# Kernel tuning notes

Measured on AMD Instinct MI355X. Metric: run time of the kernel, lower is better.

The kernel has to match this reference:

```python
import jax, jax.numpy as jnp
import numpy as np

D_MODEL = 1024
H = 16
D_K = D_MODEL // H


def setup_inputs() -> dict:
    key = jax.random.key(0)
    ks = jax.random.split(key, 12)
    B, S = 2, 2048
    q = jax.random.normal(ks[0], (B, S, D_MODEL), dtype=jnp.float32)
    k = jax.random.normal(ks[1], (B, S, D_MODEL), dtype=jnp.float32)
    v = jax.random.normal(ks[2], (B, S, D_MODEL), dtype=jnp.float32)
    mask = jax.random.randint(ks[3], (1, 1, S, S), 0, 2, dtype=jnp.int32)
    sc = 1.0 / np.sqrt(D_MODEL)
    wq = jax.random.uniform(ks[4], (D_MODEL, D_MODEL), jnp.float32, -sc, sc)
    bq = jax.random.uniform(ks[5], (D_MODEL,), jnp.float32, -sc, sc)
    wk = jax.random.uniform(ks[6], (D_MODEL, D_MODEL), jnp.float32, -sc, sc)
    bk = jax.random.uniform(ks[7], (D_MODEL,), jnp.float32, -sc, sc)
    wv = jax.random.uniform(ks[8], (D_MODEL, D_MODEL), jnp.float32, -sc, sc)
    bv = jax.random.uniform(ks[9], (D_MODEL,), jnp.float32, -sc, sc)
    wo = jax.random.uniform(ks[10], (D_MODEL, D_MODEL), jnp.float32, -sc, sc)
    bo = jax.random.uniform(ks[11], (D_MODEL,), jnp.float32, -sc, sc)
    return {"q": q, "k": k, "v": v, "mask": mask,
            "wq": wq, "bq": bq, "wk": wk, "bk": bk,
            "wv": wv, "bv": bv, "wo": wo, "bo": bo}


def reference(q, k, v, mask, wq, bq, wk, bk, wv, bv, wo, bo):
    B, S, _ = q.shape
    # linear projections (torch Linear: x @ W.T + b)
    query = q @ wq.T + bq
    key = k @ wk.T + bk
    value = v @ wv.T + bv
    # [B, S, D] -> [B, H, S, d_k]
    query = query.reshape(B, S, H, D_K).transpose(0, 2, 1, 3)
    key = key.reshape(B, S, H, D_K).transpose(0, 2, 1, 3)
    value = value.reshape(B, S, H, D_K).transpose(0, 2, 1, 3)
    scores = jnp.einsum('bhqd,bhkd->bhqk', query, key) / jnp.sqrt(
        jnp.asarray(D_K, query.dtype))
    # NOTE: source uses `-1 ** 9` which is -1 in Python, not -1e9 (soft mask)
    scores = jnp.where(mask == 0, jnp.asarray(-1.0, scores.dtype), scores)
    attn = jax.nn.softmax(scores, axis=-1)
    # source calls dropout(attn) but discards the result -> no-op
    x = jnp.einsum('bhqk,bhkd->bhqd', attn, value)
    x = x.transpose(0, 2, 1, 3).reshape(B, S, H * D_K)
    return x @ wo.T + bo
```

## Files before the change

kernel.cpp:

```cpp
#include <hip/hip_runtime.h>
#include <hip/hip_bf16.h>

#define D_MODEL 1024
#define NH 16
#define DK 64
#define S_LEN 2048
#define BATCH 2
#define M_ROWS (BATCH * S_LEN)

typedef float    floatx4 __attribute__((ext_vector_type(4)));
typedef _Float16 half8   __attribute__((ext_vector_type(8)));
typedef _Float16 half4v  __attribute__((ext_vector_type(4)));

#define LOG2E 1.4426950408889634f
#define EXPM1 0.36787944117144233f

__device__ __forceinline__ half8 ldh8(const _Float16* p) {
    return __builtin_bit_cast(half8, *(const uint4*)p);
}
__device__ __forceinline__ void gld16(const void* g, void* l) {
    __builtin_amdgcn_global_load_lds(
        (const __attribute__((address_space(1))) void*)g,
        (__attribute__((address_space(3))) void*)l, 16, 0, 0);
}
__device__ __forceinline__ float dpp_swap1(float x) {
    return __builtin_bit_cast(float,
        __builtin_amdgcn_mov_dpp(__builtin_bit_cast(int, x), 0xB1, 0xF, 0xF, false));
}
__device__ __forceinline__ void rawbar() {
    __builtin_amdgcn_sched_barrier(0);
    __builtin_amdgcn_s_barrier();
    __builtin_amdgcn_sched_barrier(0);
}

__global__ __launch_bounds__(256)
void cast_h(const float* __restrict__ s0, const float* __restrict__ s1,
            const float* __restrict__ s2, const float* __restrict__ s3,
            _Float16* __restrict__ out, int R) {
    const int z = blockIdx.y;
    const float* src = (z == 0) ? s0 : (z == 1) ? s1 : (z == 2) ? s2 : s3;
    const size_t idx = ((size_t)blockIdx.x * 256 + threadIdx.x) * 4;
    float4 v = *(const float4*)&src[idx];
    half4v h = {(_Float16)v.x, (_Float16)v.y, (_Float16)v.z, (_Float16)v.w};
    *(half4v*)&out[(size_t)z * R * 1024 + idx] = h;
}

template <int OUTMODE>
__global__ __launch_bounds__(256)
void gemm_f16(const _Float16* __restrict__ Abase, const _Float16* __restrict__ Wbase,
              const float* __restrict__ b0, const float* __restrict__ b1,
              const float* __restrict__ b2, void* __restrict__ Obase,
              void* __restrict__ Obase2) {
    __shared__ __align__(16) _Float16 As[128 * 64];
    __shared__ __align__(16) _Float16 Ws[128 * 64];
    const int tid = threadIdx.x;
    const int w = tid >> 6, lane = tid & 63;
    const int l15 = lane & 15, q4 = lane >> 4;
    const int z = (OUTMODE == 1) ? blockIdx.z : 0;
    const int m0 = blockIdx.y * 128, n0 = blockIdx.x * 128;
    const int wm = w >> 1, wn = w & 1;

    const _Float16* A = Abase + (size_t)z * M_ROWS * 1024;
    const _Float16* W = Wbase + (size_t)z * 1024 * 1024;
    const float* bias = (OUTMODE == 1) ? ((z == 0) ? b0 : (z == 1) ? b1 : b2) : b0;

    int srow[4], sseg[4];
#pragma unroll
    for (int i = 0; i < 4; i++) {
        const int slot = i * 256 + tid;
        srow[i] = slot >> 3;
        sseg[i] = ((slot & 7) ^ (srow[i] & 7)) * 8;
    }

    int aoff[4][2], woff[4][2];
#pragma unroll
    for (int r = 0; r < 4; r++) {
        const int ar = wm * 64 + r * 16 + l15;
        const int wr = wn * 64 + r * 16 + l15;
#pragma unroll
        for (int kc = 0; kc < 2; kc++) {
            aoff[r][kc] = (ar * 8 + ((kc * 4 + q4) ^ (ar & 7))) * 8;
            woff[r][kc] = (wr * 8 + ((kc * 4 + q4) ^ (wr & 7))) * 8;
        }
    }

    floatx4 acc[4][4];
#pragma unroll
    for (int r = 0; r < 4; r++)
#pragma unroll
        for (int c = 0; c < 4; c++) acc[r][c] = (floatx4){0.f, 0.f, 0.f, 0.f};

    for (int k0 = 0; k0 < 1024; k0 += 64) {
#pragma unroll
        for (int i = 0; i < 4; i++) {
            const int lb = (i * 256 + w * 64) * 8;
            gld16(&A[(size_t)(m0 + srow[i]) * 1024 + k0 + sseg[i]], &As[lb]);
            gld16(&W[(size_t)(n0 + srow[i]) * 1024 + k0 + sseg[i]], &Ws[lb]);
        }
        __syncthreads();

        half8 af[4][2], wf[4][2];
#pragma unroll
        for (int r = 0; r < 4; r++)
#pragma unroll
            for (int kc = 0; kc < 2; kc++) {
                af[r][kc] = ldh8(&As[aoff[r][kc]]);
                wf[r][kc] = ldh8(&Ws[woff[r][kc]]);
            }
#pragma unroll
        for (int kc = 0; kc < 2; kc++)
#pragma unroll
            for (int r = 0; r < 4; r++)
#pragma unroll
                for (int c = 0; c < 4; c++)
                    acc[r][c] = __builtin_amdgcn_mfma_f32_16x16x32_f16(
                        af[r][kc], wf[c][kc], acc[r][c], 0, 0, 0);
        __syncthreads();
    }

#pragma unroll
    for (int r = 0; r < 4; r++)
#pragma unroll
        for (int c = 0; c < 4; c++) {
            const int n = n0 + wn * 64 + c * 16 + l15;
            const int mbase = m0 + wm * 64 + r * 16 + q4 * 4;
            float vals[4];
#pragma unroll
            for (int reg = 0; reg < 4; reg++) vals[reg] = acc[r][c][reg] + bias[n];

            if (OUTMODE == 0) {
#pragma unroll
                for (int reg = 0; reg < 4; reg++)
                    ((float*)Obase)[(size_t)(mbase + reg) * 1024 + n] = vals[reg];
            } else if (z == 2) {
                const int b = mbase >> 11, s = mbase & 2047;
                const int h = n >> 6, d = n & 63;
                half4v hv = {(_Float16)vals[0], (_Float16)vals[1],
                             (_Float16)vals[2], (_Float16)vals[3]};
                *(half4v*)&((_Float16*)Obase2)[
                    (((size_t)((b * 16 + h) * 64 + d)) << 11) + s] = hv;
            } else {
#pragma unroll
                for (int reg = 0; reg < 4; reg++) {
                    const int m = mbase + reg;
                    float val = vals[reg];
                    if (z == 0) val *= 0.125f * LOG2E;
                    const int b = m >> 11, s = m & 2047;
                    const int h = n >> 6, d = n & 63;
                    _Float16* Oz = (_Float16*)Obase + (size_t)z * M_ROWS * 1024;
                    Oz[(((size_t)(b * 16 + h) * S_LEN + s) << 6) + d] = (_Float16)val;
                }
            }
        }
}

__global__ __launch_bounds__(256)
void mask_pack(const int* __restrict__ mask, unsigned long long* __restrict__ mb) {
    const int gw = blockIdx.x * 4 + (threadIdx.x >> 6);
    const int lane = threadIdx.x & 63;
    const int row = gw >> 5, wid = gw & 31;
    const int mv = mask[(size_t)row * S_LEN + wid * 64 + lane];
    unsigned long long bal = __ballot(mv != 0);
    if (lane == 0) mb[gw] = bal;
}

__global__ __launch_bounds__(512, 4)
void attn_mfma(const _Float16* __restrict__ Qh, const _Float16* __restrict__ Kh,
               const _Float16* __restrict__ Vt, const unsigned long long* __restrict__ mb,
               _Float16* __restrict__ Xh) {
    __shared__ __align__(16) _Float16 Ks[2][64 * 64];
    __shared__ __align__(16) _Float16 Vs[2][64 * 64];
    __shared__ __align__(16) _Float16 Ps[8][32 * 72];

    const int tid = threadIdx.x;
    const int w = tid >> 6, lane = tid & 63;
    const int z = w >> 2, w4 = w & 3;
    const int t255 = tid & 255;
    const int l15 = lane & 15, q4 = lane >> 4;
    const int bh = blockIdx.y, b = bh >> 4, h = bh & 15;
    const int qb = blockIdx.x * 128 + w4 * 32;
    const int kbase = z * 1024;

    const _Float16* Qg = Qh + ((size_t)bh * S_LEN + qb) * DK;
    const _Float16* Kg = Kh + ((size_t)bh * S_LEN + kbase) * DK;
    const _Float16* Vg = Vt + (size_t)bh * DK * S_LEN + kbase;

    half8 Aq[2][2];
#pragma unroll
    for (int qs = 0; qs < 2; qs++)
#pragma unroll
        for (int ch = 0; ch < 2; ch++)
            Aq[qs][ch] = ldh8(&Qg[(qs * 16 + l15) * DK + ch * 32 + q4 * 8]);

    int grow[2], gseg[2];
#pragma unroll
    for (int i = 0; i < 2; i++) {
        const int slot = i * 256 + t255;
        grow[i] = slot >> 3;
        gseg[i] = ((slot & 7) ^ (grow[i] & 7)) * 8;
    }

    int kb[2];
#pragma unroll
    for (int ch = 0; ch < 2; ch++)
        kb[ch] = l15 * 64 + (((ch * 4 + q4) ^ (l15 & 7)) * 8);

    const unsigned long long* mrow_p = mb + (size_t)(qb + q4 * 4) * (S_LEN / 64) + z * 16;

    floatx4 O[2][4];
#pragma unroll
    for (int qs = 0; qs < 2; qs++)
#pragma unroll
        for (int nt = 0; nt < 4; nt++) O[qs][nt] = (floatx4){0.f, 0.f, 0.f, 0.f};
    floatx4 lacc[2];
    lacc[0] = (floatx4){0.f, 0.f, 0.f, 0.f};
    lacc[1] = (floatx4){0.f, 0.f, 0.f, 0.f};

    half8 onesB;
#pragma unroll
    for (int i = 0; i < 8; i++) onesB[i] = (_Float16)1.0f;

    const bool evenlane = ((lane & 1) == 0);

#pragma unroll
    for (int i = 0; i < 2; i++) {
        const int lb = (i * 256 + w4 * 64) * 8;
        gld16(&Kg[(size_t)grow[i] * DK + gseg[i]], &Ks[z][lb]);
    }
#pragma unroll
    for (int i = 0; i < 2; i++) {
        const int lb = (i * 256 + w4 * 64) * 8;
        gld16(&Vg[(size_t)grow[i] * S_LEN + gseg[i]], &Vs[z][lb]);
    }

    for (int j0 = 0; j0 < 1024; j0 += 64) {
        const int jn = (j0 + 64) & 1023;
        const int jw = j0 >> 6;

        __builtin_amdgcn_sched_barrier(0);
        asm volatile("s_waitcnt vmcnt(2)" ::: "memory");
        rawbar();

#pragma unroll
        for (int qs = 0; qs < 2; qs++) {
            unsigned long long mw[4];
#pragma unroll
            for (int jt = 0; jt < 4; jt++) {
                floatx4 c = (floatx4){0.f, 0.f, 0.f, 0.f};
                c = __builtin_amdgcn_mfma_f32_16x16x32_f16(
                    Aq[qs][0], ldh8(&Ks[z][jt * 1024 + kb[0]]), c, 0, 0, 0);
                c = __builtin_amdgcn_mfma_f32_16x16x32_f16(
                    Aq[qs][1], ldh8(&Ks[z][jt * 1024 + kb[1]]), c, 0, 0, 0);
                if (jt == 0) {
#pragma unroll
                    for (int reg = 0; reg < 4; reg++)
                        mw[reg] = mrow_p[qs * 512 + reg * 32 + jw];
                }
#pragma unroll
                for (int reg = 0; reg < 4; reg++) {
                    const unsigned ttw =
                        (unsigned)(mw[reg] >> (jt >= 2 ? 32 : 0)) >> l15;
                    const unsigned sel = ttw & (1u << ((jt & 1) * 16));
                    float p = __builtin_amdgcn_exp2f(c[reg]);
                    p = sel ? p : EXPM1;
                    const float po = dpp_swap1(p);
                    if (evenlane) {
                        *(unsigned*)&Ps[w][(qs * 16 + q4 * 4 + reg) * 72 +
                                           jt * 16 + l15] =
                            __builtin_bit_cast(unsigned,
                                __builtin_amdgcn_cvt_pkrtz(p, po));
                    }
                }
            }
        }

        rawbar();
#pragma unroll
        for (int i = 0; i < 2; i++) {
            const int lb = (i * 256 + w4 * 64) * 8;
            gld16(&Kg[(size_t)(jn + grow[i]) * DK + gseg[i]], &Ks[z][lb]);
        }

        __builtin_amdgcn_sched_barrier(0);
        asm volatile("s_waitcnt vmcnt(2)" ::: "memory");
        rawbar();

#pragma unroll
        for (int qs = 0; qs < 2; qs++) {
            half8 Ap[2];
#pragma unroll
            for (int ch = 0; ch < 2; ch++)
                Ap[ch] = ldh8(&Ps[w][(qs * 16 + l15) * 72 + ch * 32 + q4 * 8]);
            lacc[qs] = __builtin_amdgcn_mfma_f32_16x16x32_f16(Ap[0], onesB, lacc[qs], 0, 0, 0);
            lacc[qs] = __builtin_amdgcn_mfma_f32_16x16x32_f16(Ap[1], onesB, lacc[qs], 0, 0, 0);
#pragma unroll
            for (int nt = 0; nt < 4; nt++) {
                O[qs][nt] = __builtin_amdgcn_mfma_f32_16x16x32_f16(
                    Ap[0], ldh8(&Vs[z][nt * 1024 + kb[0]]), O[qs][nt], 0, 0, 0);
                O[qs][nt] = __builtin_amdgcn_mfma_f32_16x16x32_f16(
                    Ap[1], ldh8(&Vs[z][nt * 1024 + kb[1]]), O[qs][nt], 0, 0, 0);
            }
        }

        rawbar();
#pragma unroll
        for (int i = 0; i < 2; i++) {
            const int lb = (i * 256 + w4 * 64) * 8;
            gld16(&Vg[(size_t)grow[i] * S_LEN + jn + gseg[i]], &Vs[z][lb]);
        }
    }
    __builtin_amdgcn_sched_barrier(0);

    float* Obuf = (float*)&Ps[0][0];
    if (z == 1) {
#pragma unroll
        for (int qs = 0; qs < 2; qs++)
#pragma unroll
            for (int reg = 0; reg < 4; reg++) {
                const int rl = w4 * 32 + qs * 16 + q4 * 4 + reg;
#pragma unroll
                for (int nt = 0; nt < 4; nt++)
                    Obuf[rl * 65 + nt * 16 + l15] = O[qs][nt][reg];
                if (l15 == 0) Obuf[rl * 65 + 64] = lacc[qs][reg];
            }
    }
    __syncthreads();
    if (z == 0) {
#pragma unroll
        for (int qs = 0; qs < 2; qs++)
#pragma unroll
            for (int reg = 0; reg < 4; reg++) {
                const int rl = w4 * 32 + qs * 16 + q4 * 4 + reg;
                const float inv = 1.0f / (lacc[qs][reg] + Obuf[rl * 65 + 64]);
                const int srow = qb + qs * 16 + q4 * 4 + reg;
                _Float16* Xrow = Xh + (size_t)(b * S_LEN + srow) * 1024 + h * DK;
#pragma unroll
                for (int nt = 0; nt < 4; nt++)
                    Xrow[nt * 16 + l15] =
                        (_Float16)((O[qs][nt][reg] + Obuf[rl * 65 + nt * 16 + l15]) * inv);
            }
    }
}

extern "C" void kernel_launch(void* const* d_in, const int* in_sizes, int n_in,
                              void* d_out, int out_size, void* d_ws, size_t ws_size,
                              hipStream_t stream) {
    const float* q  = (const float*)d_in[0];
    const float* k  = (const float*)d_in[1];
    const float* v  = (const float*)d_in[2];
    const int* mask = (const int*)d_in[3];
    const float* wq = (const float*)d_in[4];
    const float* bq = (const float*)d_in[5];
    const float* wk = (const float*)d_in[6];
    const float* bk = (const float*)d_in[7];
    const float* wv = (const float*)d_in[8];
    const float* bv = (const float*)d_in[9];
    const float* wo = (const float*)d_in[10];
    const float* bo = (const float*)d_in[11];
    float* out = (float*)d_out;

    char* ws = (char*)d_ws;
    const size_t MB = 1u << 20;
    _Float16* Wh   = (_Float16*)ws;
    _Float16* Ah   = (_Float16*)(ws + 8 * MB);
    _Float16* QKVh = (_Float16*)(ws + 32 * MB);
    _Float16* Vt   = (_Float16*)(ws + 56 * MB);
    unsigned long long* mb = (unsigned long long*)(ws + 64 * MB);
    _Float16* Xh   = Ah;

    cast_h<<<dim3(1024, 4), 256, 0, stream>>>(wq, wk, wv, wo, Wh, 1024);
    cast_h<<<dim3(4096, 3), 256, 0, stream>>>(q, k, v, nullptr, Ah, M_ROWS);

    gemm_f16<1><<<dim3(8, 32, 3), 256, 0, stream>>>(Ah, Wh, bq, bk, bv, QKVh, Vt);

    mask_pack<<<S_LEN * (S_LEN / 64) / 4, 256, 0, stream>>>(mask, mb);

    attn_mfma<<<dim3(16, 32), 512, 0, stream>>>(QKVh, QKVh + (size_t)M_ROWS * 1024,
                                                Vt, mb, Xh);

    gemm_f16<0><<<dim3(8, 32, 1), 256, 0, stream>>>(Xh, Wh + (size_t)3 * 1024 * 1024,
                                                    bo, bo, bo, out, nullptr);
}
```

Measured before the change: 284.9 us.

## Fuse casts and mask packing into one prep kernel; stage GEMM epilogue through LDS

After: 270.7 us. 5.0% less time.

```diff
diff --git a/kernel.cpp b/kernel.cpp
--- a/kernel.cpp
+++ b/kernel.cpp
@@ -34,15 +34,34 @@
 }
 
 __global__ __launch_bounds__(256)
-void cast_h(const float* __restrict__ s0, const float* __restrict__ s1,
-            const float* __restrict__ s2, const float* __restrict__ s3,
-            _Float16* __restrict__ out, int R) {
-    const int z = blockIdx.y;
-    const float* src = (z == 0) ? s0 : (z == 1) ? s1 : (z == 2) ? s2 : s3;
-    const size_t idx = ((size_t)blockIdx.x * 256 + threadIdx.x) * 4;
-    float4 v = *(const float4*)&src[idx];
-    half4v h = {(_Float16)v.x, (_Float16)v.y, (_Float16)v.z, (_Float16)v.w};
-    *(half4v*)&out[(size_t)z * R * 1024 + idx] = h;
+void prep(const float* __restrict__ q, const float* __restrict__ k,
+          const float* __restrict__ v, const float* __restrict__ wq,
+          const float* __restrict__ wk, const float* __restrict__ wv,
+          const float* __restrict__ wo, const int* __restrict__ mask,
+          _Float16* __restrict__ Ah, _Float16* __restrict__ Wh,
+          unsigned long long* __restrict__ mb) {
+    const int y = blockIdx.y;
+    if (y < 7) {
+        if (y >= 3 && blockIdx.x >= 1024) return;
+        const float* src = (y == 0) ? q : (y == 1) ? k : (y == 2) ? v :
+                           (y == 3) ? wq : (y == 4) ? wk : (y == 5) ? wv : wo;
+        _Float16* dst = (y < 3) ? (Ah + (size_t)y * M_ROWS * 1024)
+                                : (Wh + (size_t)(y - 3) * 1024 * 1024);
+        const size_t idx = ((size_t)blockIdx.x * 256 + threadIdx.x) * 4;
+        float4 f = *(const float4*)&src[idx];
+        half4v h = {(_Float16)f.x, (_Float16)f.y, (_Float16)f.z, (_Float16)f.w};
+        *(half4v*)&dst[idx] = h;
+    } else {
+        const int wv_ = threadIdx.x >> 6, lane = threadIdx.x & 63;
+#pragma unroll
+        for (int i = 0; i < 4; i++) {
+            const int gw = blockIdx.x * 16 + wv_ * 4 + i;
+            const int row = gw >> 5, wid = gw & 31;
+            const int mv = mask[(size_t)row * S_LEN + wid * 64 + lane];
+            unsigned long long bal = __ballot(mv != 0);
+            if (lane == 0) mb[gw] = bal;
+        }
+    }
 }
 
 template <int OUTMODE>
@@ -51,8 +70,9 @@
               const float* __restrict__ b0, const float* __restrict__ b1,
               const float* __restrict__ b2, void* __restrict__ Obase,
               void* __restrict__ Obase2) {
-    __shared__ __align__(16) _Float16 As[128 * 64];
-    __shared__ __align__(16) _Float16 Ws[128 * 64];
+    __shared__ __align__(16) _Float16 SM[16384];
+    _Float16* As = SM;
+    _Float16* Ws = SM + 8192;
     const int tid = threadIdx.x;
     const int w = tid >> 6, lane = tid & 63;
     const int l15 = lane & 15, q4 = lane >> 4;
@@ -118,50 +138,77 @@
         __syncthreads();
     }
 
-#pragma unroll
-    for (int r = 0; r < 4; r++)
-#pragma unroll
-        for (int c = 0; c < 4; c++) {
-            const int n = n0 + wn * 64 + c * 16 + l15;
-            const int mbase = m0 + wm * 64 + r * 16 + q4 * 4;
-            float vals[4];
-#pragma unroll
-            for (int reg = 0; reg < 4; reg++) vals[reg] = acc[r][c][reg] + bias[n];
-
-            if (OUTMODE == 0) {
+    if (OUTMODE == 0) {
+#pragma unroll
+        for (int r = 0; r < 4; r++)
+#pragma unroll
+            for (int c = 0; c < 4; c++) {
+                const int n = n0 + wn * 64 + c * 16 + l15;
+                const int mbase = m0 + wm * 64 + r * 16 + q4 * 4;
 #pragma unroll
                 for (int reg = 0; reg < 4; reg++)
-                    ((float*)Obase)[(size_t)(mbase + reg) * 1024 + n] = vals[reg];
-            } else if (z == 2) {
-                const int b = mbase >> 11, s = mbase & 2047;
-                const int h = n >> 6, d = n & 63;
-                half4v hv = {(_Float16)vals[0], (_Float16)vals[1],
-                             (_Float16)vals[2], (_Float16)vals[3]};
-                *(half4v*)&((_Float16*)Obase2)[
-                    (((size_t)((b * 16 + h) * 64 + d)) << 11) + s] = hv;
-            } else {
-#pragma unroll
-                for (int reg = 0; reg < 4; reg++) {
-                    const int m = mbase + reg;
-                    float val = vals[reg];
-                    if (z == 0) val *= 0.125f * LOG2E;
-                    const int b = m >> 11, s = m & 2047;
-                    const int h = n >> 6, d = n & 63;
-                    _Float16* Oz = (_Float16*)Obase + (size_t)z * M_ROWS * 1024;
-                    Oz[(((size_t)(b * 16 + h) * S_LEN + s) << 6) + d] = (_Float16)val;
+                    ((float*)Obase)[(size_t)(mbase + reg) * 1024 + n] =
+                        acc[r][c][reg] + bias[n];
+            }
+    } else {
+        const int h0 = n0 >> 6;
+        const int bB = m0 >> 11;
+        if (z == 2) {
+#pragma unroll
+            for (int r = 0; r < 4; r++)
+#pragma unroll
+                for (int c = 0; c < 4; c++) {
+                    const int nl = wn * 64 + c * 16 + l15;
+                    const int ml = wm * 64 + r * 16 + q4 * 4;
+                    half4v hv;
+#pragma unroll
+                    for (int reg = 0; reg < 4; reg++)
+                        hv[reg] = (_Float16)(acc[r][c][reg] + bias[n0 + nl]);
+                    const int seg = ml >> 3, wi = ml & 7;
+                    *(half4v*)&SM[nl * 128 + ((seg ^ (nl & 7)) << 3) + wi] = hv;
                 }
-            }
-        }
-}
-
-__global__ __launch_bounds__(256)
-void mask_pack(const int* __restrict__ mask, unsigned long long* __restrict__ mb) {
-    const int gw = blockIdx.x * 4 + (threadIdx.x >> 6);
-    const int lane = threadIdx.x & 63;
-    const int row = gw >> 5, wid = gw & 31;
-    const int mv = mask[(size_t)row * S_LEN + wid * 64 + lane];
-    unsigned long long bal = __ballot(mv != 0);
-    if (lane == 0) mb[gw] = bal;
+            __syncthreads();
+#pragma unroll
+            for (int it = 0; it < 8; it++) {
+                const int chunk = it * 256 + tid;
+                const int row = chunk >> 4, seg = chunk & 15;
+                half8 v8 = ldh8(&SM[row * 128 + ((seg ^ (row & 7)) << 3)]);
+                const int d = row & 63, hh = row >> 6;
+                const int s = (m0 & 2047) + seg * 8;
+                *(uint4*)&((_Float16*)Obase2)[
+                    (((size_t)((bB * 16 + h0 + hh) * 64 + d)) << 11) + s] =
+                    __builtin_bit_cast(uint4, v8);
+            }
+        } else {
+            const float sc = (z == 0) ? 0.125f * LOG2E : 1.0f;
+#pragma unroll
+            for (int r = 0; r < 4; r++)
+#pragma unroll
+                for (int c = 0; c < 4; c++) {
+                    const int nl = wn * 64 + c * 16 + l15;
+                    const int seg = nl >> 3, wi = nl & 7;
+                    const float bv = bias[n0 + nl];
+#pragma unroll
+                    for (int reg = 0; reg < 4; reg++) {
+                        const int ml = wm * 64 + r * 16 + q4 * 4 + reg;
+                        SM[ml * 128 + ((seg ^ (ml & 7)) << 3) + wi] =
+                            (_Float16)((acc[r][c][reg] + bv) * sc);
+                    }
+                }
+            __syncthreads();
+            _Float16* Oz = (_Float16*)Obase + (size_t)z * M_ROWS * 1024;
+#pragma unroll
+            for (int it = 0; it < 8; it++) {
+                const int chunk = it * 256 + tid;
+                const int row = chunk >> 4, seg = chunk & 15;
+                half8 v8 = ldh8(&SM[row * 128 + ((seg ^ (row & 7)) << 3)]);
+                const int s = (m0 + row) & 2047;
+                const int hh = seg >> 3, d = (seg & 7) * 8;
+                *(uint4*)&Oz[(((size_t)((bB * 16 + h0 + hh)) * S_LEN + s) << 6) + d] =
+                    __builtin_bit_cast(uint4, v8);
+            }
+        }
+    }
 }
 
 __global__ __launch_bounds__(512, 4)
@@ -247,10 +294,12 @@
 #pragma unroll
             for (int jt = 0; jt < 4; jt++) {
                 floatx4 c = (floatx4){0.f, 0.f, 0.f, 0.f};
+                __builtin_amdgcn_s_setprio(1);
                 c = __builtin_amdgcn_mfma_f32_16x16x32_f16(
                     Aq[qs][0], ldh8(&Ks[z][jt * 1024 + kb[0]]), c, 0, 0, 0);
                 c = __builtin_amdgcn_mfma_f32_16x16x32_f16(
                     Aq[qs][1], ldh8(&Ks[z][jt * 1024 + kb[1]]), c, 0, 0, 0);
+                __builtin_amdgcn_s_setprio(0);
                 if (jt == 0) {
 #pragma unroll
                     for (int reg = 0; reg < 4; reg++)
@@ -291,6 +340,7 @@
 #pragma unroll
             for (int ch = 0; ch < 2; ch++)
                 Ap[ch] = ldh8(&Ps[w][(qs * 16 + l15) * 72 + ch * 32 + q4 * 8]);
+            __builtin_amdgcn_s_setprio(1);
             lacc[qs] = __builtin_amdgcn_mfma_f32_16x16x32_f16(Ap[0], onesB, lacc[qs], 0, 0, 0);
             lacc[qs] = __builtin_amdgcn_mfma_f32_16x16x32_f16(Ap[1], onesB, lacc[qs], 0, 0, 0);
 #pragma unroll
@@ -300,6 +350,7 @@
                 O[qs][nt] = __builtin_amdgcn_mfma_f32_16x16x32_f16(
                     Ap[1], ldh8(&Vs[z][nt * 1024 + kb[1]]), O[qs][nt], 0, 0, 0);
             }
+            __builtin_amdgcn_s_setprio(0);
         }
 
         rawbar();
@@ -368,12 +419,10 @@
     unsigned long long* mb = (unsigned long long*)(ws + 64 * MB);
     _Float16* Xh   = Ah;
 
-    cast_h<<<dim3(1024, 4), 256, 0, stream>>>(wq, wk, wv, wo, Wh, 1024);
-    cast_h<<<dim3(4096, 3), 256, 0, stream>>>(q, k, v, nullptr, Ah, M_ROWS);
+    prep<<<dim3(4096, 8), 256, 0, stream>>>(q, k, v, wq, wk, wv, wo, mask,
+                                            Ah, Wh, mb);
 
     gemm_f16<1><<<dim3(8, 32, 3), 256, 0, stream>>>(Ah, Wh, bq, bk, bv, QKVh, Vt);
-
-    mask_pack<<<S_LEN * (S_LEN / 64) / 4, 256, 0, stream>>>(mask, mb);
 
     attn_mfma<<<dim3(16, 32), 512, 0, stream>>>(QKVh, QKVh + (size_t)M_ROWS * 1024,
                                                 Vt, mb, Xh);
```
